# Performance work log

Hardware: AMD Instinct MI355X
Metric: run time of the kernel (lower is better)

The kernel has to match this reference:

```python
import jax, jax.numpy as jnp
import numpy as np

PAD = 1  # module padding

def setup_inputs() -> dict:
    key = jax.random.key(0)
    k1, k2 = jax.random.split(key)
    x = jax.random.normal(k1, (1, 256, 512, 512), dtype=jnp.float32)
    # module uses uniform(-xavier, xavier) with xavier = 1/sqrt(kh*kw)
    xavier = 1.0 / np.sqrt(3 * 3)
    weight = jax.random.uniform(k2, (256, 256, 3, 3), dtype=jnp.float32,
                                minval=-xavier, maxval=xavier)
    return {"x": x, "weight": weight}

def reference(x, weight):
    # Stride-1 cross-correlation with zero padding PAD, matching the
    # module's per-pixel slice*kernel sum (batch must be 1 for that code).
    return jax.lax.conv_general_dilated(
        x, weight,
        window_strides=(1, 1),
        padding=[(PAD, PAD), (PAD, PAD)],
        dimension_numbers=("NCHW", "OIHW", "NCHW"),
    )
```

## Files before the change

### kernel.cpp

```cpp
#include <hip/hip_runtime.h>
#include <stdint.h>

typedef __attribute__((ext_vector_type(8))) __bf16 bf16x8;
typedef __attribute__((ext_vector_type(16))) float f32x16;

constexpr int CIN = 256, COUT = 256, HH = 512, WW = 512;
constexpr int BC = 16;
constexpr int NCB = CIN / BC;
constexpr int MT = 128;
constexpr int TY = 8, TX = 32;

__device__ __forceinline__ unsigned short f2bf(float f) {
    union { float f; unsigned int u; } v; v.f = f;
    return (unsigned short)((v.u + 0x7fffu + ((v.u >> 16) & 1u)) >> 16);
}

__device__ __align__(256) unsigned short g_zero16[16] = {};

__device__ __forceinline__ void gload16(const void* g, const void* l) {
    __builtin_amdgcn_global_load_lds(
        (const __attribute__((address_space(1))) unsigned int*)g,
        (__attribute__((address_space(3))) unsigned int*)l, 16, 0, 0);
}

__global__ void wt_transform2(const float* __restrict__ w, unsigned short* __restrict__ wt2) {
    const int cbtap = blockIdx.x;
    const int cb = cbtap / 9, tap = cbtap - cb * 9;
    #pragma unroll 4
    for (int e = threadIdx.x; e < 4096; e += 256) {
        const int k = e >> 4, ci = e & 15;
        wt2[cbtap * 4096 + e] = f2bf(w[(k * CIN + cb * BC + ci) * 9 + tap]);
    }
}

__global__ __launch_bounds__(256)
void x_transform(const float* __restrict__ x, unsigned short* __restrict__ xb) {
    __shared__ __align__(16) float Xl[16][72];
    const int b   = blockIdx.x;
    const int y   = b >> 5;
    const int xc  = (b >> 2) & 7;
    const int cbg = b & 3;
    const int x0  = xc * 64;
    const int tid = threadIdx.x;
    const int ci  = tid >> 4, p4 = (tid & 15) << 2;
    const int px  = tid >> 2, cig = tid & 3;
    #pragma unroll 1
    for (int g = 0; g < 4; ++g) {
        const int cb = cbg * 4 + g;
        const float4 v = *reinterpret_cast<const float4*>(
            x + ((long long)(cb * 16 + ci) * HH + y) * WW + x0 + p4);
        *reinterpret_cast<float4*>(&Xl[ci][p4]) = v;
        __syncthreads();
        ushort4 o;
        o.x = f2bf(Xl[cig * 4 + 0][px]);
        o.y = f2bf(Xl[cig * 4 + 1][px]);
        o.z = f2bf(Xl[cig * 4 + 2][px]);
        o.w = f2bf(Xl[cig * 4 + 3][px]);
        *reinterpret_cast<ushort4*>(
            xb + (((long long)cb * HH + y) * WW + x0 + px) * 16 + cig * 4) = o;
        __syncthreads();
    }
}

__global__ __launch_bounds__(256, 2)
void conv_mfma3(const unsigned short* __restrict__ xb, const unsigned short* __restrict__ wt2,
                float* __restrict__ out) {
    __shared__ __align__(16) unsigned short Wl[9][MT][16];
    __shared__ __align__(16) unsigned short Xs[TY + 2][36][16];

    const int bid = blockIdx.x;
    const int swz = ((bid & 7) << 8) | (bid >> 3);
    const int k0 = (swz & 1) * MT;
    const int tile = swz >> 1;
    const int x0 = (tile & 15) * TX;
    const int y0 = (tile >> 4) * TY;

    const int tid = threadIdx.x;
    const int lane = tid & 63;
    const int wave = tid >> 6;
    const int wm = wave & 1;
    const int wn = wave >> 1;
    const int ln31 = lane & 31;
    const int lh8 = (lane >> 5) * 8;

    f32x16 acc[2][4];
    #pragma unroll
    for (int i = 0; i < 2; ++i)
        #pragma unroll
        for (int j = 0; j < 4; ++j)
            #pragma unroll
            for (int r = 0; r < 16; ++r) acc[i][j][r] = 0.f;

    const unsigned short* wsrc0 = wt2 + (size_t)k0 * 16 + (size_t)tid * 8;
    unsigned short* wl = ((unsigned short*)Wl) + (tid >> 6) * 512;

    {
        const unsigned short* wsrc = wsrc0;
        #pragma unroll
        for (int i = 0; i < 9; ++i)
            gload16(wsrc + (size_t)i * 4096, wl + i * 2048);
        #pragma unroll
        for (int t = 0; t < 3; ++t) {
            const int rr = wave + t * 4;
            if (rr < TY + 2) {
                const int yy = y0 - 1 + rr;
                const bool rok = (unsigned)yy < (unsigned)HH;
                const size_t rowb = ((size_t)0 * HH + (rok ? yy : 0)) * WW;
                const int gx = x0 - 1 + (lane >> 1);
                const bool ok = rok && ((unsigned)gx < (unsigned)WW);
                const unsigned short* gs = ok ? xb + (rowb + gx) * 16 + (lane & 1) * 8 : g_zero16;
                gload16(gs, &Xs[rr][0][0]);
                if (lane < 8) {
                    const int gx2 = x0 + 31 + (lane >> 1);
                    const bool ok2 = rok && gx2 < WW;
                    const unsigned short* gs2 = ok2 ? xb + (rowb + gx2) * 16 + (lane & 1) * 8 : g_zero16;
                    gload16(gs2, &Xs[rr][32][0]);
                }
            }
        }
        asm volatile("s_waitcnt vmcnt(0)" ::: "memory");
        __builtin_amdgcn_s_barrier();
    }

    for (int cb = 0; cb < NCB; ++cb) {
        #pragma unroll
        for (int s = 0; s < 3; ++s) {
            #pragma unroll
            for (int rr = 0; rr < 3; ++rr) {
                const int tap = rr * 3 + s;
                const bf16x8 a0 = *reinterpret_cast<const bf16x8*>(&Wl[tap][wm * 64 + ln31][lh8]);
                const bf16x8 a1 = *reinterpret_cast<const bf16x8*>(&Wl[tap][wm * 64 + 32 + ln31][lh8]);
                #pragma unroll
                for (int j = 0; j < 4; ++j) {
                    const bf16x8 b = *reinterpret_cast<const bf16x8*>(&Xs[wn * 4 + j + rr][s + ln31][lh8]);
                    acc[0][j] = __builtin_amdgcn_mfma_f32_32x32x16_bf16(a0, b, acc[0][j], 0, 0, 0);
                    acc[1][j] = __builtin_amdgcn_mfma_f32_32x32x16_bf16(a1, b, acc[1][j], 0, 0, 0);
                }
            }
        }

        if (cb + 1 < NCB) {
            const int cn = cb + 1;
            asm volatile("s_waitcnt lgkmcnt(0)" ::: "memory");
            __builtin_amdgcn_s_barrier();
            const unsigned short* wsrc = wsrc0 + (size_t)cn * 9 * 4096;
            #pragma unroll
            for (int i = 0; i < 9; ++i)
                gload16(wsrc + (size_t)i * 4096, wl + i * 2048);
            #pragma unroll
            for (int t = 0; t < 3; ++t) {
                const int rr = wave + t * 4;
                if (rr < TY + 2) {
                    const int yy = y0 - 1 + rr;
                    const bool rok = (unsigned)yy < (unsigned)HH;
                    const size_t rowb = ((size_t)cn * HH + (rok ? yy : 0)) * WW;
                    const int gx = x0 - 1 + (lane >> 1);
                    const bool ok = rok && ((unsigned)gx < (unsigned)WW);
                    const unsigned short* gs = ok ? xb + (rowb + gx) * 16 + (lane & 1) * 8 : g_zero16;
                    gload16(gs, &Xs[rr][0][0]);
                    if (lane < 8) {
                        const int gx2 = x0 + 31 + (lane >> 1);
                        const bool ok2 = rok && gx2 < WW;
                        const unsigned short* gs2 = ok2 ? xb + (rowb + gx2) * 16 + (lane & 1) * 8 : g_zero16;
                        gload16(gs2, &Xs[rr][32][0]);
                    }
                }
            }
            asm volatile("s_waitcnt vmcnt(0)" ::: "memory");
            __builtin_amdgcn_s_barrier();
        }
    }

    #pragma unroll
    for (int i = 0; i < 2; ++i) {
        const int mb = k0 + wm * 64 + i * 32 + (lane >> 5) * 4;
        #pragma unroll
        for (int j = 0; j < 4; ++j) {
            const long long py = y0 + wn * 4 + j;
            const long long px = x0 + ln31;
            #pragma unroll
            for (int r = 0; r < 16; ++r) {
                const int m = mb + (r & 3) + 8 * (r >> 2);
                out[((long long)m * HH + py) * WW + px] = acc[i][j][r];
            }
        }
    }
}

__global__ void conv_naive(const float* __restrict__ x, const float* __restrict__ w,
                           float* __restrict__ out) {
    const int k = blockIdx.x;
    const int y = blockIdx.y;
    const int xx = blockIdx.z * 256 + threadIdx.x;
    float a = 0.f;
    for (int c = 0; c < CIN; ++c) {
        const float* wp = w + ((k * CIN + c) * 9);
        const float* xp = x + (long long)c * HH * WW;
        #pragma unroll
        for (int r = 0; r < 3; ++r) {
            const int yy = y + r - 1;
            if ((unsigned)yy >= (unsigned)HH) continue;
            const float* row = xp + (long long)yy * WW;
            #pragma unroll
            for (int s = 0; s < 3; ++s) {
                const int gx = xx + s - 1;
                const float v = ((unsigned)gx < (unsigned)WW) ? row[gx] : 0.f;
                a += wp[r * 3 + s] * v;
            }
        }
    }
    out[((long long)k * HH + y) * WW + xx] = a;
}

extern "C" void kernel_launch(void* const* d_in, const int* in_sizes, int n_in,
                              void* d_out, int out_size, void* d_ws, size_t ws_size,
                              hipStream_t stream) {
    const float* x = (const float*)d_in[0];
    const float* w = (const float*)d_in[1];
    float* out = (float*)d_out;

    const size_t xb_bytes  = (size_t)NCB * HH * WW * BC * sizeof(unsigned short);
    const size_t wt2_bytes = (size_t)144 * 4096 * sizeof(unsigned short);

    if (ws_size >= xb_bytes + wt2_bytes) {
        unsigned short* xb  = (unsigned short*)d_ws;
        unsigned short* wt2 = (unsigned short*)d_ws + xb_bytes / sizeof(unsigned short);
        x_transform<<<16384, 256, 0, stream>>>(x, xb);
        wt_transform2<<<144, 256, 0, stream>>>(w, wt2);
        conv_mfma3<<<2048, 256, 0, stream>>>(xb, wt2, out);
    } else {
        conv_naive<<<dim3(256, 512, 2), 256, 0, stream>>>(x, w, out);
    }
}
```

Baseline: 692.3 us.

## Double-buffer LDS stages and enlarge the conv tile to 12 rows

Moves the conv kernel to double-buffered weight and input tiles in LDS, so loads for the next channel block are issued before computing the current one. The old scheme loaded after the compute and stalled on them. Each block now covers 12 output rows instead of 8, and each wave loads its input rows into registers once and reuses them across the three vertical taps, raising MFMA work per LDS load. In exchange, occupancy drops to one block per CU because of the larger LDS footprint and accumulators. The 1376-block grid also no longer divides evenly into waves, which adds tail imbalance and a partial last row tile that needs guarded stores.

```diff
diff --git a/kernel.cpp b/kernel.cpp
--- a/kernel.cpp
+++ b/kernel.cpp
@@ -8,7 +8,8 @@
 constexpr int BC = 16;
 constexpr int NCB = CIN / BC;
 constexpr int MT = 128;
-constexpr int TY = 8, TX = 32;
+constexpr int TY = 12, TX = 32;
+constexpr int XROWS = TY + 2;
 
 __device__ __forceinline__ unsigned short f2bf(float f) {
     union { float f; unsigned int u; } v; v.f = f;
@@ -62,14 +63,14 @@
     }
 }
 
-__global__ __launch_bounds__(256, 2)
-void conv_mfma3(const unsigned short* __restrict__ xb, const unsigned short* __restrict__ wt2,
+__global__ __launch_bounds__(256, 1)
+void conv_mfma4(const unsigned short* __restrict__ xb, const unsigned short* __restrict__ wt2,
                 float* __restrict__ out) {
-    __shared__ __align__(16) unsigned short Wl[9][MT][16];
-    __shared__ __align__(16) unsigned short Xs[TY + 2][36][16];
+    __shared__ __align__(16) unsigned short Wl[2][9][MT][16];
+    __shared__ __align__(16) unsigned short Xs[2][XROWS][36][16];
 
     const int bid = blockIdx.x;
-    const int swz = ((bid & 7) << 8) | (bid >> 3);
+    const int swz = (bid & 7) * 172 + (bid >> 3);
     const int k0 = (swz & 1) * MT;
     const int tile = swz >> 1;
     const int x0 = (tile & 15) * TX;
@@ -83,105 +84,88 @@
     const int ln31 = lane & 31;
     const int lh8 = (lane >> 5) * 8;
 
-    f32x16 acc[2][4];
+    f32x16 acc[2][6];
     #pragma unroll
     for (int i = 0; i < 2; ++i)
         #pragma unroll
-        for (int j = 0; j < 4; ++j)
+        for (int j = 0; j < 6; ++j)
             #pragma unroll
             for (int r = 0; r < 16; ++r) acc[i][j][r] = 0.f;
 
     const unsigned short* wsrc0 = wt2 + (size_t)k0 * 16 + (size_t)tid * 8;
-    unsigned short* wl = ((unsigned short*)Wl) + (tid >> 6) * 512;
-
-    {
-        const unsigned short* wsrc = wsrc0;
+
+    auto STAGE = [&](int cbn, int bufn) {
+        const unsigned short* ws = wsrc0 + (size_t)cbn * 9 * 4096;
+        unsigned short* wld = &Wl[bufn][0][0][0] + wave * 512;
         #pragma unroll
         for (int i = 0; i < 9; ++i)
-            gload16(wsrc + (size_t)i * 4096, wl + i * 2048);
-        #pragma unroll
-        for (int t = 0; t < 3; ++t) {
-            const int rr = wave + t * 4;
-            if (rr < TY + 2) {
-                const int yy = y0 - 1 + rr;
-                const bool rok = (unsigned)yy < (unsigned)HH;
-                const size_t rowb = ((size_t)0 * HH + (rok ? yy : 0)) * WW;
+            gload16(ws + (size_t)i * 4096, wld + i * 2048);
+        #pragma unroll
+        for (int k = 0; k < 7; ++k) {
+            const int slot = wave * 7 + k;
+            const int row = slot >> 1, part = slot & 1;
+            const int yy = y0 - 1 + row;
+            const bool rok = (unsigned)yy < (unsigned)HH;
+            const size_t rowb = ((size_t)cbn * HH + (rok ? yy : 0)) * WW;
+            if (part == 0) {
                 const int gx = x0 - 1 + (lane >> 1);
                 const bool ok = rok && ((unsigned)gx < (unsigned)WW);
                 const unsigned short* gs = ok ? xb + (rowb + gx) * 16 + (lane & 1) * 8 : g_zero16;
-                gload16(gs, &Xs[rr][0][0]);
-                if (lane < 8) {
-                    const int gx2 = x0 + 31 + (lane >> 1);
-                    const bool ok2 = rok && gx2 < WW;
-                    const unsigned short* gs2 = ok2 ? xb + (rowb + gx2) * 16 + (lane & 1) * 8 : g_zero16;
-                    gload16(gs2, &Xs[rr][32][0]);
+                gload16(gs, &Xs[bufn][row][0][0]);
+            } else if (lane < 4) {
+                const int gx2 = x0 + 31 + (lane >> 1);
+                const bool ok2 = rok && gx2 < WW;
+                const unsigned short* gs2 = ok2 ? xb + (rowb + gx2) * 16 + (lane & 1) * 8 : g_zero16;
+                gload16(gs2, &Xs[bufn][row][32][0]);
+            }
+        }
+    };
+
+    STAGE(0, 0);
+    asm volatile("s_waitcnt vmcnt(0)" ::: "memory");
+    __builtin_amdgcn_s_barrier();
+
+    #pragma unroll 2
+    for (int cb = 0; cb < NCB; ++cb) {
+        const int cur = cb & 1;
+        if (cb + 1 < NCB) STAGE(cb + 1, cur ^ 1);
+
+        #pragma unroll
+        for (int s = 0; s < 3; ++s) {
+            bf16x8 b[8];
+            #pragma unroll
+            for (int o = 0; o < 8; ++o)
+                b[o] = *reinterpret_cast<const bf16x8*>(&Xs[cur][wn * 6 + o][s + ln31][lh8]);
+            #pragma unroll
+            for (int rr = 0; rr < 3; ++rr) {
+                const int tap = rr * 3 + s;
+                const bf16x8 a0 = *reinterpret_cast<const bf16x8*>(&Wl[cur][tap][wm * 64 + ln31][lh8]);
+                const bf16x8 a1 = *reinterpret_cast<const bf16x8*>(&Wl[cur][tap][wm * 64 + 32 + ln31][lh8]);
+                #pragma unroll
+                for (int j = 0; j < 6; ++j) {
+                    acc[0][j] = __builtin_amdgcn_mfma_f32_32x32x16_bf16(a0, b[j + rr], acc[0][j], 0, 0, 0);
+                    acc[1][j] = __builtin_amdgcn_mfma_f32_32x32x16_bf16(a1, b[j + rr], acc[1][j], 0, 0, 0);
                 }
             }
         }
+
         asm volatile("s_waitcnt vmcnt(0)" ::: "memory");
         __builtin_amdgcn_s_barrier();
-    }
-
-    for (int cb = 0; cb < NCB; ++cb) {
-        #pragma unroll
-        for (int s = 0; s < 3; ++s) {
-            #pragma unroll
-            for (int rr = 0; rr < 3; ++rr) {
-                const int tap = rr * 3 + s;
-                const bf16x8 a0 = *reinterpret_cast<const bf16x8*>(&Wl[tap][wm * 64 + ln31][lh8]);
-                const bf16x8 a1 = *reinterpret_cast<const bf16x8*>(&Wl[tap][wm * 64 + 32 + ln31][lh8]);
-                #pragma unroll
-                for (int j = 0; j < 4; ++j) {
-                    const bf16x8 b = *reinterpret_cast<const bf16x8*>(&Xs[wn * 4 + j + rr][s + ln31][lh8]);
-                    acc[0][j] = __builtin_amdgcn_mfma_f32_32x32x16_bf16(a0, b, acc[0][j], 0, 0, 0);
-                    acc[1][j] = __builtin_amdgcn_mfma_f32_32x32x16_bf16(a1, b, acc[1][j], 0, 0, 0);
-                }
-            }
-        }
-
-        if (cb + 1 < NCB) {
-            const int cn = cb + 1;
-            asm volatile("s_waitcnt lgkmcnt(0)" ::: "memory");
-            __builtin_amdgcn_s_barrier();
-            const unsigned short* wsrc = wsrc0 + (size_t)cn * 9 * 4096;
-            #pragma unroll
-            for (int i = 0; i < 9; ++i)
-                gload16(wsrc + (size_t)i * 4096, wl + i * 2048);
-            #pragma unroll
-            for (int t = 0; t < 3; ++t) {
-                const int rr = wave + t * 4;
-                if (rr < TY + 2) {
-                    const int yy = y0 - 1 + rr;
-                    const bool rok = (unsigned)yy < (unsigned)HH;
-                    const size_t rowb = ((size_t)cn * HH + (rok ? yy : 0)) * WW;
-                    const int gx = x0 - 1 + (lane >> 1);
-                    const bool ok = rok && ((unsigned)gx < (unsigned)WW);
-                    const unsigned short* gs = ok ? xb + (rowb + gx) * 16 + (lane & 1) * 8 : g_zero16;
-                    gload16(gs, &Xs[rr][0][0]);
-                    if (lane < 8) {
-                        const int gx2 = x0 + 31 + (lane >> 1);
-                        const bool ok2 = rok && gx2 < WW;
-                        const unsigned short* gs2 = ok2 ? xb + (rowb + gx2) * 16 + (lane & 1) * 8 : g_zero16;
-                        gload16(gs2, &Xs[rr][32][0]);
-                    }
-                }
-            }
-            asm volatile("s_waitcnt vmcnt(0)" ::: "memory");
-            __builtin_amdgcn_s_barrier();
-        }
     }
 
     #pragma unroll
     for (int i = 0; i < 2; ++i) {
         const int mb = k0 + wm * 64 + i * 32 + (lane >> 5) * 4;
         #pragma unroll
-        for (int j = 0; j < 4; ++j) {
-            const long long py = y0 + wn * 4 + j;
-            const long long px = x0 + ln31;
-            #pragma unroll
-            for (int r = 0; r < 16; ++r) {
-                const int m = mb + (r & 3) + 8 * (r >> 2);
-                out[((long long)m * HH + py) * WW + px] = acc[i][j][r];
+        for (int j = 0; j < 6; ++j) {
+            const int py = y0 + wn * 6 + j;
+            if (py < HH) {
+                const long long px = x0 + ln31;
+                #pragma unroll
+                for (int r = 0; r < 16; ++r) {
+                    const int m = mb + (r & 3) + 8 * (r >> 2);
+                    out[((long long)m * HH + py) * WW + px] = acc[i][j][r];
+                }
             }
         }
     }
@@ -227,7 +211,7 @@
         unsigned short* wt2 = (unsigned short*)d_ws + xb_bytes / sizeof(unsigned short);
         x_transform<<<16384, 256, 0, stream>>>(x, xb);
         wt_transform2<<<144, 256, 0, stream>>>(w, wt2);
-        conv_mfma3<<<2048, 256, 0, stream>>>(xb, wt2, out);
+        conv_mfma4<<<1376, 256, 0, stream>>>(xb, wt2, out);
     } else {
         conv_naive<<<dim3(256, 512, 2), 256, 0, stream>>>(x, w, out);
     }
```

Measured after the change: 725.8 us. +4.8%, slower.
